# Optimization experiments

Measured on AMD Instinct MI355X. Metric: run time of the kernel, lower is better.

## Reference

```python
import jax, jax.numpy as jnp
import numpy as np

EPS = 1e-8  # torch.nn.CosineSimilarity default eps


def setup_inputs() -> dict:
    key = jax.random.key(0)
    k1, k2 = jax.random.split(key)
    B, D = 2048, 512
    return {
        "z_i": jax.random.normal(k1, (B, D), dtype=jnp.float32),
        "z_j": jax.random.normal(k2, (B, D), dtype=jnp.float32),
        "temperature": 0.5,
    }


def _neg_mask_indices(B):
    # static (numpy) mask: remove diagonal and the two +/-B positive diagonals
    N = 2 * B
    mask = np.ones((N, N), dtype=bool)
    np.fill_diagonal(mask, False)
    idx = np.arange(B)
    mask[idx, idx + B] = False
    mask[idx + B, idx] = False
    rows, cols = np.where(mask)  # each row keeps exactly N-2 entries, row-major order
    return rows, cols


def reference(z_i, z_j, temperature):
    B = z_i.shape[0]
    N = 2 * B
    z = jnp.concatenate([z_i, z_j], axis=0)                      # [N, D]
    # cosine similarity = normalized GEMM (same math as pairwise CosineSimilarity)
    zn = z / jnp.maximum(jnp.linalg.norm(z, axis=1, keepdims=True), EPS)
    sim = jnp.matmul(zn, zn.T) / temperature                      # [N, N]

    pos = jnp.concatenate([jnp.diagonal(sim, B), jnp.diagonal(sim, -B)])[:, None]  # [N, 1]
    rows, cols = _neg_mask_indices(B)
    neg = sim[rows, cols].reshape(N, N - 2)                       # [N, N-2]

    logits = jnp.concatenate([pos, neg], axis=1)                  # [N, N-1], label = 0
    # sum-reduced cross-entropy with label 0, divided by N
    loss = jnp.sum(jax.nn.logsumexp(logits, axis=1) - logits[:, 0]) / N

    # avg_rank: position of the positive (column 0) in descending sort of logits
    order = jnp.argsort(-logits, axis=1)
    avg_rank = jnp.mean(jnp.argmin(order, axis=1).astype(jnp.float32))
    return loss, avg_rank
```

## Files before the change

kernel.cpp:

```cpp
#include <hip/hip_runtime.h>
#include <math.h>

#define DDIM 512
#define THREADS 256
#define BT 128
#define BK 64
#define NT 32
#define NCH 64

typedef __attribute__((ext_vector_type(8))) __bf16 bf16x8;
typedef __attribute__((ext_vector_type(4))) float f32x4;
typedef __attribute__((ext_vector_type(8))) unsigned short ushort8;

__device__ __forceinline__ float bf2f(unsigned short u) {
  union { unsigned int i; float f; } v; v.i = ((unsigned int)u) << 16; return v.f;
}
__device__ __forceinline__ unsigned short f2bf(float f) {
  unsigned int u = __builtin_bit_cast(unsigned int, f);
  return (unsigned short)((u + 0x7fffu + ((u >> 16) & 1u)) >> 16);
}

#define GLOAD_LDS16(gp, lp)                                                   \
  __builtin_amdgcn_global_load_lds(                                           \
      (const __attribute__((address_space(1))) unsigned int*)(gp),            \
      (__attribute__((address_space(3))) unsigned int*)(lp), 16, 0, 0)

__global__ void k_prep(const float* __restrict__ zi, const float* __restrict__ zj,
                       const float* __restrict__ tempp,
                       unsigned short* __restrict__ znb, float* __restrict__ pos,
                       int B) {
  int wv = (blockIdx.x * blockDim.x + threadIdx.x) >> 6;
  int lane = threadIdx.x & 63;
  if (wv >= B) return;
  const float* a = zi + (size_t)wv * DDIM;
  const float* b = zj + (size_t)wv * DDIM;
  float4 a0 = *(const float4*)(a + lane * 8);
  float4 a1 = *(const float4*)(a + lane * 8 + 4);
  float4 b0 = *(const float4*)(b + lane * 8);
  float4 b1 = *(const float4*)(b + lane * 8 + 4);
  float av[8] = {a0.x, a0.y, a0.z, a0.w, a1.x, a1.y, a1.z, a1.w};
  float bv[8] = {b0.x, b0.y, b0.z, b0.w, b1.x, b1.y, b1.z, b1.w};
  float sa = 0.f, sb = 0.f;
#pragma unroll
  for (int i = 0; i < 8; ++i) { sa = fmaf(av[i], av[i], sa); sb = fmaf(bv[i], bv[i], sb); }
#pragma unroll
  for (int off = 32; off; off >>= 1) { sa += __shfl_xor(sa, off, 64); sb += __shfl_xor(sb, off, 64); }
  float ia = 1.f / fmaxf(sqrtf(sa), 1e-8f);
  float ib = 1.f / fmaxf(sqrtf(sb), 1e-8f);
  ushort8 ua, ub;
  float fa[8], fb[8];
#pragma unroll
  for (int i = 0; i < 8; ++i) {
    unsigned short x = f2bf(av[i] * ia); ua[i] = x; fa[i] = bf2f(x);
    unsigned short y = f2bf(bv[i] * ib); ub[i] = y; fb[i] = bf2f(y);
  }
  *(ushort8*)(znb + (size_t)wv * DDIM + lane * 8) = ua;
  *(ushort8*)(znb + (size_t)(wv + B) * DDIM + lane * 8) = ub;
  float pd = 0.f;
#pragma unroll
  for (int i = 0; i < 8; ++i) pd = fmaf(fa[i], fb[i], pd);
#pragma unroll
  for (int off = 32; off; off >>= 1) pd += __shfl_xor(pd, off, 64);
  if (lane == 0) {
    float p = pd / tempp[0];
    pos[wv] = p; pos[wv + B] = p;
  }
}

__device__ __forceinline__ void stage_tile(const unsigned short* __restrict__ znb,
                                           int panel0, int k0, unsigned char* dst,
                                           int wave, int lane) {
  const int srow_in = lane >> 3;
  const int slog = (lane & 7) ^ srow_in;
#pragma unroll
  for (int j = 0; j < 4; ++j) {
    const int ww = wave * 4 + j;
    const int row = 8 * ww + srow_in;
    GLOAD_LDS16(znb + (size_t)(panel0 + row) * DDIM + k0 + slog * 8, dst + ww * 1024);
  }
}

__global__ __launch_bounds__(THREADS) void k_main(
    const unsigned short* __restrict__ znb, const float* __restrict__ pos,
    const float* __restrict__ tempp, float* __restrict__ partS,
    float* __restrict__ partC, int B) {
  int l = blockIdx.x;
  int bi = 0;
  while (l >= NT - bi) { l -= NT - bi; ++bi; }
  const int bj = bi + l;
  const int r0 = bi * BT, c0 = bj * BT;
  const bool diag = (bi == bj);
  const float invt = 1.0f / tempp[0];

  __shared__ __align__(16) unsigned char sA[2][BT * BK * 2];
  __shared__ __align__(16) unsigned char sB[2][BT * BK * 2];

  const int t = threadIdx.x;
  const int lane = t & 63;
  const int wave = t >> 6;
  const int wr = wave >> 1, wc = wave & 1;
  const int cl = lane & 15, g = lane >> 4;

  f32x4 acc[4][4];
#pragma unroll
  for (int m = 0; m < 4; ++m)
#pragma unroll
    for (int n = 0; n < 4; ++n) acc[m][n] = (f32x4){0.f, 0.f, 0.f, 0.f};

  stage_tile(znb, r0, 0, sA[0], wave, lane);
  if (!diag) stage_tile(znb, c0, 0, sB[0], wave, lane);
  __syncthreads();

  for (int kt = 0; kt < DDIM / BK; ++kt) {
    const int cur = kt & 1;
    if (kt < DDIM / BK - 1) {
      stage_tile(znb, r0, (kt + 1) * BK, sA[cur ^ 1], wave, lane);
      if (!diag) stage_tile(znb, c0, (kt + 1) * BK, sB[cur ^ 1], wave, lane);
    }
    const unsigned char* pA = sA[cur];
    const unsigned char* pB = diag ? sA[cur] : sB[cur];
#pragma unroll
    for (int ks = 0; ks < 2; ++ks) {
      const int phys = (g + ks * 4) ^ (cl & 7);
      bf16x8 aF[4], bF[4];
#pragma unroll
      for (int m = 0; m < 4; ++m)
        aF[m] = *(const bf16x8*)(pA + (wr * 64 + m * 16 + cl) * 128 + phys * 16);
#pragma unroll
      for (int n = 0; n < 4; ++n)
        bF[n] = *(const bf16x8*)(pB + (wc * 64 + n * 16 + cl) * 128 + phys * 16);
#pragma unroll
      for (int m = 0; m < 4; ++m)
#pragma unroll
        for (int n = 0; n < 4; ++n)
          acc[m][n] = __builtin_amdgcn_mfma_f32_16x16x32_bf16(aF[m], bF[n], acc[m][n], 0, 0, 0);
    }
    __syncthreads();
  }

  int growv[16], gpartr[16];
  float pvr[16];
#pragma unroll
  for (int m = 0; m < 4; ++m)
#pragma unroll
    for (int reg = 0; reg < 4; ++reg) {
      int idx = m * 4 + reg;
      int grow = r0 + wr * 64 + m * 16 + g * 4 + reg;
      growv[idx] = grow;
      gpartr[idx] = (grow < B) ? grow + B : grow - B;
      pvr[idx] = pos[grow];
    }
  int gcolv[4], gpartc[4];
  float pvc[4];
#pragma unroll
  for (int n = 0; n < 4; ++n) {
    int gcol = c0 + wc * 64 + n * 16 + cl;
    gcolv[n] = gcol;
    gpartc[n] = (gcol < B) ? gcol + B : gcol - B;
    pvc[n] = pos[gcol];
  }

  float ssr[16], ccr[16], ssc[4], ccc[4];
#pragma unroll
  for (int i = 0; i < 16; ++i) { ssr[i] = 0.f; ccr[i] = 0.f; }
#pragma unroll
  for (int n = 0; n < 4; ++n) { ssc[n] = 0.f; ccc[n] = 0.f; }

#pragma unroll
  for (int m = 0; m < 4; ++m)
#pragma unroll
    for (int n = 0; n < 4; ++n)
#pragma unroll
      for (int reg = 0; reg < 4; ++reg) {
        const int idx = m * 4 + reg;
        float val = acc[m][n][reg] * invt;
        float e = __expf(val);
        bool isd = diag && (gcolv[n] == growv[idx]);
        if (!isd) {
          ssr[idx] += e;
          ccr[idx] += (gcolv[n] != gpartr[idx] && val > pvr[idx]) ? 1.f : 0.f;
        }
        if (!diag) {
          ssc[n] += e;
          ccc[n] += (growv[idx] != gpartc[n] && val > pvc[n]) ? 1.f : 0.f;
        }
      }

  const int chR = bj * 2 + wc;
#pragma unroll
  for (int idx = 0; idx < 16; ++idx) {
    float s = ssr[idx], c = ccr[idx];
#pragma unroll
    for (int off = 1; off < 16; off <<= 1) {
      s += __shfl_xor(s, off, 64);
      c += __shfl_xor(c, off, 64);
    }
    if (cl == 0) {
      partS[(size_t)growv[idx] * NCH + chR] = s;
      partC[(size_t)growv[idx] * NCH + chR] = c;
    }
  }
  if (!diag) {
    const int chC = bi * 2 + wr;
#pragma unroll
    for (int n = 0; n < 4; ++n) {
      float s = ssc[n], c = ccc[n];
      s += __shfl_xor(s, 16, 64); c += __shfl_xor(c, 16, 64);
      s += __shfl_xor(s, 32, 64); c += __shfl_xor(c, 32, 64);
      if (g == 0) {
        partS[(size_t)gcolv[n] * NCH + chC] = s;
        partC[(size_t)gcolv[n] * NCH + chC] = c;
      }
    }
  }
}

__global__ void k_rowfin(const float* __restrict__ partS, const float* __restrict__ partC,
                         const float* __restrict__ pos, float* __restrict__ rowL,
                         float* __restrict__ rowC, int N) {
  int r = (blockIdx.x * blockDim.x + threadIdx.x) >> 6;
  int lane = threadIdx.x & 63;
  if (r >= N) return;
  float s = partS[(size_t)r * NCH + lane];
  float c = partC[(size_t)r * NCH + lane];
#pragma unroll
  for (int off = 32; off; off >>= 1) { s += __shfl_xor(s, off, 64); c += __shfl_xor(c, off, 64); }
  if (lane == 0) {
    rowL[r] = logf(s) - pos[r];
    rowC[r] = c;
  }
}

__global__ void k_final(const float* __restrict__ rowL, const float* __restrict__ rowC,
                        float* __restrict__ out, int N) {
  float ls = 0.f, cs = 0.f;
  for (int r = threadIdx.x; r < N; r += THREADS) { ls += rowL[r]; cs += rowC[r]; }
  __shared__ float l[THREADS], c[THREADS];
  l[threadIdx.x] = ls; c[threadIdx.x] = cs;
  __syncthreads();
  for (int off = THREADS / 2; off; off >>= 1) {
    if (threadIdx.x < off) { l[threadIdx.x] += l[threadIdx.x + off]; c[threadIdx.x] += c[threadIdx.x + off]; }
    __syncthreads();
  }
  if (threadIdx.x == 0) { out[0] = l[0] / (float)N; out[1] = c[0] / (float)N; }
}

extern "C" void kernel_launch(void* const* d_in, const int* in_sizes, int n_in,
                              void* d_out, int out_size, void* d_ws, size_t ws_size,
                              hipStream_t stream) {
  const float* zi = (const float*)d_in[0];
  const float* zj = (const float*)d_in[1];
  const float* temp = (const float*)d_in[2];
  float* out = (float*)d_out;

  const int B = in_sizes[0] / DDIM;
  const int N = 2 * B;

  unsigned short* znb = (unsigned short*)d_ws;
  float* fws = (float*)(znb + (size_t)N * DDIM);
  float* pos   = fws;
  float* partS = pos + N;
  float* partC = partS + (size_t)N * NCH;
  float* rowL  = partC + (size_t)N * NCH;
  float* rowC  = rowL + N;

  k_prep<<<(B * 64) / THREADS, THREADS, 0, stream>>>(zi, zj, temp, znb, pos, B);
  const int ntiles = NT * (NT + 1) / 2;
  k_main<<<ntiles, THREADS, 0, stream>>>(znb, pos, temp, partS, partC, B);
  k_rowfin<<<(N * 64) / THREADS, THREADS, 0, stream>>>(partS, partC, pos, rowL, rowC, N);
  k_final<<<1, THREADS, 0, stream>>>(rowL, rowC, out, N);
}
```

Before: 50.89 us.

## Load MFMA fragments directly from global memory instead of LDS staging

Removes the double-buffered LDS staging (global_load_lds plus barriers) in the GEMM tile kernel. Each wave now reads its bf16 A/B fragments straight from global memory, which is expected to hit L2 because the data is small (4096x512 bf16). This drops the LDS traffic and per-k-step syncs and frees LDS for occupancy. In exchange, waves in a block reload overlapping rows redundantly, and the global loads are strided 16-byte accesses with no cross-wave sharing.

Result: slower. 81.56 us (+60.3%).

```diff
diff --git a/kernel.cpp b/kernel.cpp
--- a/kernel.cpp
+++ b/kernel.cpp
@@ -4,7 +4,6 @@
 #define DDIM 512
 #define THREADS 256
 #define BT 128
-#define BK 64
 #define NT 32
 #define NCH 64
 
@@ -19,11 +18,6 @@
   unsigned int u = __builtin_bit_cast(unsigned int, f);
   return (unsigned short)((u + 0x7fffu + ((u >> 16) & 1u)) >> 16);
 }
-
-#define GLOAD_LDS16(gp, lp)                                                   \
-  __builtin_amdgcn_global_load_lds(                                           \
-      (const __attribute__((address_space(1))) unsigned int*)(gp),            \
-      (__attribute__((address_space(3))) unsigned int*)(lp), 16, 0, 0)
 
 __global__ void k_prep(const float* __restrict__ zi, const float* __restrict__ zj,
                        const float* __restrict__ tempp,
@@ -67,19 +61,6 @@
   }
 }
 
-__device__ __forceinline__ void stage_tile(const unsigned short* __restrict__ znb,
-                                           int panel0, int k0, unsigned char* dst,
-                                           int wave, int lane) {
-  const int srow_in = lane >> 3;
-  const int slog = (lane & 7) ^ srow_in;
-#pragma unroll
-  for (int j = 0; j < 4; ++j) {
-    const int ww = wave * 4 + j;
-    const int row = 8 * ww + srow_in;
-    GLOAD_LDS16(znb + (size_t)(panel0 + row) * DDIM + k0 + slog * 8, dst + ww * 1024);
-  }
-}
-
 __global__ __launch_bounds__(THREADS) void k_main(
     const unsigned short* __restrict__ znb, const float* __restrict__ pos,
     const float* __restrict__ tempp, float* __restrict__ partS,
@@ -92,9 +73,6 @@
   const bool diag = (bi == bj);
   const float invt = 1.0f / tempp[0];
 
-  __shared__ __align__(16) unsigned char sA[2][BT * BK * 2];
-  __shared__ __align__(16) unsigned char sB[2][BT * BK * 2];
-
   const int t = threadIdx.x;
   const int lane = t & 63;
   const int wave = t >> 6;
@@ -107,35 +85,24 @@
 #pragma unroll
     for (int n = 0; n < 4; ++n) acc[m][n] = (f32x4){0.f, 0.f, 0.f, 0.f};
 
-  stage_tile(znb, r0, 0, sA[0], wave, lane);
-  if (!diag) stage_tile(znb, c0, 0, sB[0], wave, lane);
-  __syncthreads();
-
-  for (int kt = 0; kt < DDIM / BK; ++kt) {
-    const int cur = kt & 1;
-    if (kt < DDIM / BK - 1) {
-      stage_tile(znb, r0, (kt + 1) * BK, sA[cur ^ 1], wave, lane);
-      if (!diag) stage_tile(znb, c0, (kt + 1) * BK, sB[cur ^ 1], wave, lane);
-    }
-    const unsigned char* pA = sA[cur];
-    const unsigned char* pB = diag ? sA[cur] : sB[cur];
-#pragma unroll
-    for (int ks = 0; ks < 2; ++ks) {
-      const int phys = (g + ks * 4) ^ (cl & 7);
-      bf16x8 aF[4], bF[4];
-#pragma unroll
-      for (int m = 0; m < 4; ++m)
-        aF[m] = *(const bf16x8*)(pA + (wr * 64 + m * 16 + cl) * 128 + phys * 16);
+  const unsigned short* baseA = znb + (size_t)(r0 + wr * 64 + cl) * DDIM + g * 8;
+  const unsigned short* baseB = znb + (size_t)(c0 + wc * 64 + cl) * DDIM + g * 8;
+
+#pragma unroll 2
+  for (int kt = 0; kt < DDIM / 32; ++kt) {
+    const int kk = kt * 32;
+    bf16x8 aF[4], bF[4];
+#pragma unroll
+    for (int m = 0; m < 4; ++m)
+      aF[m] = *(const bf16x8*)(baseA + (size_t)(m * 16) * DDIM + kk);
+#pragma unroll
+    for (int n = 0; n < 4; ++n)
+      bF[n] = *(const bf16x8*)(baseB + (size_t)(n * 16) * DDIM + kk);
+#pragma unroll
+    for (int m = 0; m < 4; ++m)
 #pragma unroll
       for (int n = 0; n < 4; ++n)
-        bF[n] = *(const bf16x8*)(pB + (wc * 64 + n * 16 + cl) * 128 + phys * 16);
-#pragma unroll
-      for (int m = 0; m < 4; ++m)
-#pragma unroll
-        for (int n = 0; n < 4; ++n)
-          acc[m][n] = __builtin_amdgcn_mfma_f32_16x16x32_bf16(aF[m], bF[n], acc[m][n], 0, 0, 0);
-    }
-    __syncthreads();
+        acc[m][n] = __builtin_amdgcn_mfma_f32_16x16x32_bf16(aF[m], bF[n], acc[m][n], 0, 0, 0);
   }
 
   int growv[16], gpartr[16];
```

## Single-buffer LDS, raise occupancy hint, and remap tile order across XCDs

Applied to the files above, without the earlier changes.

Removes double-buffering of the A/B LDS tiles, halving shared memory per block, and adds a min-blocks-per-CU launch bound of 4 so more blocks can be resident. Global-to-LDS loads now complete before each k-step's compute, with a barrier between, so latency is meant to be hidden by occupancy instead of prefetching. Block indices are permuted by blockIdx&7 so consecutive tiles spread across the eight XCDs. The risk is exposed load latency per k-step if occupancy does not rise enough, plus register pressure from the launch bound.

Result: no change. 50.63 us (-0.5%).

```diff
diff --git a/kernel.cpp b/kernel.cpp
--- a/kernel.cpp
+++ b/kernel.cpp
@@ -6,6 +6,7 @@
 #define BT 128
 #define BK 64
 #define NT 32
+#define NTILES (NT * (NT + 1) / 2)
 #define NCH 64
 
 typedef __attribute__((ext_vector_type(8))) __bf16 bf16x8;
@@ -80,20 +81,20 @@
   }
 }
 
-__global__ __launch_bounds__(THREADS) void k_main(
+__global__ __launch_bounds__(THREADS, 4) void k_main(
     const unsigned short* __restrict__ znb, const float* __restrict__ pos,
     const float* __restrict__ tempp, float* __restrict__ partS,
     float* __restrict__ partC, int B) {
-  int l = blockIdx.x;
+  int tri = (blockIdx.x & 7) * (NTILES / 8) + (blockIdx.x >> 3);
   int bi = 0;
-  while (l >= NT - bi) { l -= NT - bi; ++bi; }
-  const int bj = bi + l;
+  while (tri >= NT - bi) { tri -= NT - bi; ++bi; }
+  const int bj = bi + tri;
   const int r0 = bi * BT, c0 = bj * BT;
   const bool diag = (bi == bj);
   const float invt = 1.0f / tempp[0];
 
-  __shared__ __align__(16) unsigned char sA[2][BT * BK * 2];
-  __shared__ __align__(16) unsigned char sB[2][BT * BK * 2];
+  __shared__ __align__(16) unsigned char sA[BT * BK * 2];
+  __shared__ __align__(16) unsigned char sB[BT * BK * 2];
 
   const int t = threadIdx.x;
   const int lane = t & 63;
@@ -107,18 +108,13 @@
 #pragma unroll
     for (int n = 0; n < 4; ++n) acc[m][n] = (f32x4){0.f, 0.f, 0.f, 0.f};
 
-  stage_tile(znb, r0, 0, sA[0], wave, lane);
-  if (!diag) stage_tile(znb, c0, 0, sB[0], wave, lane);
-  __syncthreads();
-
   for (int kt = 0; kt < DDIM / BK; ++kt) {
-    const int cur = kt & 1;
-    if (kt < DDIM / BK - 1) {
-      stage_tile(znb, r0, (kt + 1) * BK, sA[cur ^ 1], wave, lane);
-      if (!diag) stage_tile(znb, c0, (kt + 1) * BK, sB[cur ^ 1], wave, lane);
-    }
-    const unsigned char* pA = sA[cur];
-    const unsigned char* pB = diag ? sA[cur] : sB[cur];
+    stage_tile(znb, r0, kt * BK, sA, wave, lane);
+    if (!diag) stage_tile(znb, c0, kt * BK, sB, wave, lane);
+    __syncthreads();
+
+    const unsigned char* pA = sA;
+    const unsigned char* pB = diag ? sA : sB;
 #pragma unroll
     for (int ks = 0; ks < 2; ++ks) {
       const int phys = (g + ks * 4) ^ (cl & 7);
@@ -135,7 +131,8 @@
         for (int n = 0; n < 4; ++n)
           acc[m][n] = __builtin_amdgcn_mfma_f32_16x16x32_bf16(aF[m], bF[n], acc[m][n], 0, 0, 0);
     }
-    __syncthreads();
+    if (kt + 1 < DDIM / BK)
+      __syncthreads();
   }
 
   int growv[16], gpartr[16];
@@ -265,8 +262,7 @@
   float* rowC  = rowL + N;
 
   k_prep<<<(B * 64) / THREADS, THREADS, 0, stream>>>(zi, zj, temp, znb, pos, B);
-  const int ntiles = NT * (NT + 1) / 2;
-  k_main<<<ntiles, THREADS, 0, stream>>>(znb, pos, temp, partS, partC, B);
+  k_main<<<NTILES, THREADS, 0, stream>>>(znb, pos, temp, partS, partC, B);
   k_rowfin<<<(N * 64) / THREADS, THREADS, 0, stream>>>(partS, partC, pos, rowL, rowC, N);
   k_final<<<1, THREADS, 0, stream>>>(rowL, rowC, out, N);
 }
```
